# Performance work log

Hardware: AMD Instinct MI355X
Metric: run time of the kernel (lower is better)

The kernel has to match this reference:

```python
import jax, jax.numpy as jnp
import numpy as np

B, D, WIN, SW = 256, 38, 640, 10
S = WIN // SW  # 64 time steps
EPS = 1e-5

def leaky(v):
    return jnp.where(v > 0, v, 0.01 * v)

def _ln(v, g, b):
    mu = v.mean(-1, keepdims=True)
    var = v.var(-1, keepdims=True)
    return g * (v - mu) / jnp.sqrt(var + EPS) + b

def setup_inputs():
    key = jax.random.key(0)
    ks = jax.random.split(key, 24)
    n = lambda k, shp, s=0.05: jax.random.normal(k, shp, jnp.float32) * s
    return {
        'x': jax.random.normal(ks[0], (B, D, WIN), jnp.float32),
        'W1': n(ks[1], (D, 64, SW)), 'b1': n(ks[2], (D, 64)),
        'W2': n(ks[3], (D, 4, 3)), 'b2': n(ks[4], (D, 4)),
        'Wl': n(ks[5], (D, 64, 124)), 'bl': n(ks[6], (D, 64)),
        'Wb1': n(ks[7], (64, 64)), 'bb1': n(ks[8], (64,)),
        'lng': jnp.ones((64,), jnp.float32), 'lnb': jnp.zeros((64,), jnp.float32),
        'Wb2': n(ks[9], (64, 64)), 'bb2': n(ks[10], (64,)),
        'Wq': n(ks[11], (1, 64)), 'bq': n(ks[12], (1,)),
        'Wk': n(ks[13], (D, 64)), 'bk': n(ks[14], (D,)),
        'Wv1': n(ks[15], (D, 32, 64)), 'bv1': n(ks[16], (D, 32)),
        'lnvg': jnp.ones((D, 32), jnp.float32), 'lnvb': jnp.zeros((D, 32), jnp.float32),
        'Wv2': n(ks[17], (D, 32)), 'bv2': n(ks[18], (D,)),
        'Wq2': n(ks[19], (1, 64 * D)), 'bq2': n(ks[20], (1,)),
        'Wk2': n(ks[21], (S, 64 * D)), 'bk2': n(ks[22], (S,)),
    }

def reference(x, W1, b1, W2, b2, Wl, bl, Wb1, bb1, lng, lnb, Wb2, bb2,
              Wq, bq, Wk, bk, Wv1, bv1, lnvg, lnvb, Wv2, bv2, Wq2, bq2, Wk2, bk2):
    Bsz = x.shape[0]
    # FE1: per-channel Conv1d(1,64,k=SW,stride=SW) == window-reshape + per-dim GEMM
    xw = x.reshape(Bsz, D, S, SW)
    f1 = leaky(jnp.einsum('bdsw,dow->bdso', xw, W1) + b1[None, :, None, :])  # [B,D,S,64]
    # FE2: per-channel Conv1d(1,4,k=3,p=1) over the 64 features
    xp = jnp.pad(f1, ((0, 0), (0, 0), (0, 0), (1, 1)))
    win = jnp.stack([xp[..., r:r + 64] for r in range(3)], -1)  # [B,D,S,64,3]
    c = leaky(jnp.einsum('bdstr,dcr->bdsct', win, W2) + b2[None, :, None, :, None])  # [B,D,S,4,64]
    # MaxPool1d(3, stride=2): 64 -> 31
    m = jnp.max(jnp.stack([c[..., s:s + 61:2] for s in range(3)], 0), 0)  # [B,D,S,4,31]
    e = leaky(jnp.einsum('bdsf,dof->bdso', m.reshape(Bsz, D, S, 124), Wl) + bl[None, :, None, :])  # embed [B,D,S,64]
    # BeforeInstanceEncoder (shared), recurrent accumulator == cumsum over time
    h = leaky(_ln(jnp.einsum('bdso,po->bdsp', e, Wb1) + bb1, lng, lnb))
    g = leaky(jnp.einsum('bdsp,qp->bdsq', h, Wb2) + bb2)
    acml = jnp.cumsum(g, axis=2)  # [B,D,S,64]
    wq = jax.nn.sigmoid(jnp.einsum('bdso,o->bds', e, Wq[0]) + bq[0])            # [B,D,S]
    wk = jax.nn.sigmoid(jnp.einsum('bdso,jo->bdsj', acml, Wk) + bk)             # [B,D,S,D]
    att1 = jax.nn.softmax(jnp.einsum('bks,bjsk->bsj', wq, wk) / np.float32(np.sqrt(D)), axis=-1)  # [B,S,D]
    v = leaky(_ln(jnp.einsum('bdso,dho->bdsh', e, Wv1) + bv1[None, :, None, :],
                  lnvg[None, :, None, :], lnvb[None, :, None, :]))
    wv = jax.nn.relu(jnp.einsum('bdsh,dh->bds', v, Wv2) + bv2[None, :, None])   # [B,D,S]
    cont1 = jnp.transpose(wv, (0, 2, 1)) * att1  # [B,S,D]
    contributes1 = cont1[..., None]              # [B,S,D,1]
    output1 = cont1.sum(-1, keepdims=True)       # [B,S,1]
    # bag-level attention over time
    ef = jnp.transpose(e, (0, 2, 1, 3)).reshape(Bsz, S, D * 64)
    wq_a = jax.nn.sigmoid(ef @ Wq2.T + bq2)[..., 0]  # [B,S]
    wk_a = jax.nn.sigmoid(ef @ Wk2.T + bk2)          # [B,S,S]
    att2 = jax.nn.softmax(jnp.einsum('bs,bts->bt', wq_a, wk_a) / np.float32(np.sqrt(WIN)), axis=-1)  # [B,S]
    contributes2 = output1 * att2[..., None]  # [B,S,1]
    output2 = contributes2.sum(1)             # [B,1]
    return (output2, contributes2, contributes1)
```

## Files before the change

### kernel.cpp

```cpp
#include <hip/hip_runtime.h>
#include <math.h>

#define Bv 256
#define Dv 38
#define Sv 64
#define SWv 10
#define EPSv 1e-5f

typedef float f4 __attribute__((ext_vector_type(4)));

__device__ __forceinline__ float leaky(float v){ return v > 0.f ? v : 0.01f*v; }
__device__ __forceinline__ float sigm(float v){ return 1.f/(1.f+expf(-v)); }

__device__ __forceinline__ float wred64(float v){
  #pragma unroll
  for (int off=32; off; off>>=1) v += __shfl_xor(v, off, 64);
  return v;
}
__device__ __forceinline__ float wmax64(float v){
  #pragma unroll
  for (int off=32; off; off>>=1) v = fmaxf(v, __shfl_xor(v, off, 64));
  return v;
}

__global__ __launch_bounds__(256) void k0_pack(
    const float* __restrict__ Wl, const float* __restrict__ W1,
    const float* __restrict__ Wv1, const float* __restrict__ Wb1,
    const float* __restrict__ Wb2, const float* __restrict__ Wk,
    const float* __restrict__ Wk2,
    float* __restrict__ wlT, float* __restrict__ w1T, float* __restrict__ wv1T,
    float* __restrict__ wb1T, float* __restrict__ wb2T, float* __restrict__ wkT,
    float* __restrict__ wk2T)
{
  int idx = blockIdx.x*256 + threadIdx.x;
  if (idx < 330752) {
    int d = idx / 8704, r = idx % 8704;
    int c = r / 1088, rr = r % 1088;
    int q = rr / 68, o = rr % 68;
    int ch = q >> 2, io = q & 3, fi = 4*c + io;
    float v = 0.f;
    if (o < 64 && fi <= 30) v = Wl[d*7936 + o*124 + ch*31 + fi];
    wlT[idx] = v;
  } else if (idx < 356592) {
    int t = idx - 330752;
    int d = t / 680, rr = t % 680;
    int w = rr / 68, o = rr % 68;
    w1T[t] = (o < 64) ? W1[d*640 + o*10 + w] : 0.f;
  } else if (idx < 444144) {
    int t = idx - 356592;
    int d = t / 2304, rr = t % 2304;
    int o = rr / 36, h = rr % 36;
    wv1T[t] = (h < 32) ? Wv1[d*2048 + h*64 + o] : 0.f;
  } else if (idx < 448240) {
    int t = idx - 444144;
    int o = t >> 6, p = t & 63;
    wb1T[t] = Wb1[p*64 + o];
  } else if (idx < 452336) {
    int t = idx - 448240;
    int p = t >> 6, q = t & 63;
    wb2T[t] = Wb2[q*64 + p];
  } else if (idx < 454896) {
    int t = idx - 452336;
    int q = t / 40, k = t % 40;
    wkT[t] = (k < Dv) ? Wk[k*64 + q] : 0.f;
  } else if (idx < 610544) {
    int t = idx - 454896;
    int d = t / 4096, rr = t % 4096;
    int o = rr >> 6, s = rr & 63;
    wk2T[t] = Wk2[s*2432 + d*64 + o];
  }
}

__global__ __launch_bounds__(256, 3) void k1_fe4(
    const float* __restrict__ x,
    const float* __restrict__ w1T_all, const float* __restrict__ b1,
    const float* __restrict__ W2, const float* __restrict__ b2,
    const float* __restrict__ wlT_all, const float* __restrict__ bl,
    const float* __restrict__ Wq, const float* __restrict__ bq,
    const float* __restrict__ wv1T_all, const float* __restrict__ bv1,
    const float* __restrict__ lnvg, const float* __restrict__ lnvb,
    const float* __restrict__ Wv2, const float* __restrict__ bv2,
    const float* __restrict__ Wq2,
    float* __restrict__ e_wsT, float* __restrict__ wq2_ws, float* __restrict__ wv_ws,
    float* __restrict__ wqa_p)
{
  __shared__ float sm[12688];
  const int d  = blockIdx.x >> 7;
  const int b0 = (blockIdx.x & 127) * 2;
  const int tid = threadIdx.x;
  const int z = tid >> 7;
  const int t = tid & 127;
  const int tx = t & 15, ty = t >> 4;
  const int wz = ty >> 2;
  const int bd = (b0 + z)*Dv + d;
  const float bq0 = bq[0];

#define PJ(j) ((j) < 4 ? 4*ty + (j) : 32 + 4*ty + ((j)-4))

  if (tid < 64) {
    sm[12032+tid] = b1[d*64+tid];
    sm[12096+tid] = bl[d*64+tid];
    sm[12160+tid] = Wq[tid];
    sm[12368+tid] = Wq2[d*64+tid];
  } else if (tid < 96) {
    int u = tid-64;
    sm[12240+u]=bv1[d*32+u]; sm[12272+u]=lnvg[d*32+u];
    sm[12304+u]=lnvb[d*32+u]; sm[12336+u]=Wv2[d*32+u];
  } else if (tid < 108) sm[12224+(tid-96)] = W2[d*12+(tid-96)];
  else if (tid < 112)   sm[12236+(tid-108)] = b2[d*4+(tid-108)];

  {
    const f4* s4 = (const f4*)(w1T_all + (size_t)d*680);
    if (tid < 170) ((f4*)&sm[9792])[tid] = s4[tid];
  }
  for (int i = tid; i < 1280; i += 256) {
    int z2 = i / 640, tt = i % 640;
    sm[10472 + z2*680 + (tt%10)*68 + tt/10] =
      x[((size_t)((b0+z2)*Dv + d))*640 + tt];
  }
  const f4* wlsrc = (const f4*)(wlT_all + (size_t)d*8704);
  {
    ((f4*)&sm[8704])[tid] = wlsrc[tid];
    if (tid < 16) ((f4*)&sm[8704])[tid+256] = wlsrc[tid+256];
  }
  __syncthreads();

  float fe[4][8];
  #pragma unroll
  for (int i=0;i<4;++i)
    #pragma unroll
    for (int j=0;j<8;++j) fe[i][j]=0.f;
  #pragma unroll
  for (int w = 0; w < 10; ++w) {
    f4 a   = *(const f4*)&sm[10472 + z*680 + w*68 + 4*tx];
    f4 blo = *(const f4*)&sm[9792 + w*68 + 4*ty];
    f4 bhi = *(const f4*)&sm[9792 + w*68 + 32 + 4*ty];
    #pragma unroll
    for (int i=0;i<4;++i)
      #pragma unroll
      for (int j=0;j<8;++j) fe[i][j] += a[i]*((j<4)?blo[j&3]:bhi[j&3]);
  }
  #pragma unroll
  for (int j=0;j<8;++j) {
    int o = PJ(j);
    float bb = sm[12032+o];
    f4 v = {leaky(fe[0][j]+bb), leaky(fe[1][j]+bb), leaky(fe[2][j]+bb), leaky(fe[3][j]+bb)};
    *(f4*)&sm[z*4352 + o*68 + 4*tx] = v;
  }
  __syncthreads();

  float ea[4][8];
  #pragma unroll
  for (int i=0;i<4;++i)
    #pragma unroll
    for (int j=0;j<8;++j) ea[i][j]=0.f;

  f4 wr0, wr1;
  for (int c = 0; c < 8; ++c) {
    if (c > 0) {
      ((f4*)&sm[8704])[tid] = wr0;
      if (tid < 16) ((f4*)&sm[8704])[tid+256] = wr1;
    }
    {
      int sg = t & 15, io = (t >> 4) & 3, chh = t >> 6;
      int fi = 4*c + io;
      if (fi <= 30) {
        int t0 = 2*fi - 1;
        const float* fsrc = &sm[z*4352];
        f4 v0;
        if (fi == 0) { v0[0]=0.f; v0[1]=0.f; v0[2]=0.f; v0[3]=0.f; }
        else         { v0 = *(const f4*)&fsrc[t0*68 + 4*sg]; }
        f4 v1 = *(const f4*)&fsrc[(t0+1)*68 + 4*sg];
        f4 v2 = *(const f4*)&fsrc[(t0+2)*68 + 4*sg];
        f4 v3 = *(const f4*)&fsrc[(t0+3)*68 + 4*sg];
        f4 v4 = *(const f4*)&fsrc[(t0+4)*68 + 4*sg];
        float* mdst = &sm[9792 + z*1088];
        #pragma unroll
        for (int cc2 = 0; cc2 < 2; ++cc2) {
          int ch = 2*chh + cc2;
          float w0=sm[12224+ch*3], w1=sm[12224+ch*3+1], w2=sm[12224+ch*3+2];
          float bb=sm[12236+ch];
          f4 r;
          #pragma unroll
          for (int e2=0;e2<4;++e2) {
            float ca = bb + v0[e2]*w0 + v1[e2]*w1 + v2[e2]*w2;
            float cb = bb + v1[e2]*w0 + v2[e2]*w1 + v3[e2]*w2;
            float cc = bb + v2[e2]*w0 + v3[e2]*w1 + v4[e2]*w2;
            r[e2] = fmaxf(fmaxf(leaky(ca),leaky(cb)),leaky(cc));
          }
          *(f4*)&mdst[(ch*4+io)*68 + 4*sg] = r;
        }
      }
    }
    if (c < 7) {
      wr0 = wlsrc[(c+1)*272 + tid];
      if (tid < 16) wr1 = wlsrc[(c+1)*272 + 256 + tid];
    }
    __syncthreads();
    {
      const float* ma = &sm[9792 + z*1088];
      #pragma unroll
      for (int q=0;q<16;++q){
        f4 a   = *(const f4*)&ma[q*68+4*tx];
        f4 blo = *(const f4*)&sm[8704 + q*68+4*ty];
        f4 bhi = *(const f4*)&sm[8704 + q*68+32+4*ty];
        #pragma unroll
        for (int i=0;i<4;++i)
          #pragma unroll
          for (int j=0;j<8;++j) ea[i][j] += a[i]*((j<4)?blo[j&3]:bhi[j&3]);
      }
    }
    __syncthreads();
  }

  float ev[4][8];
  #pragma unroll
  for (int i=0;i<4;++i)
    #pragma unroll
    for (int j=0;j<8;++j) ev[i][j] = leaky(ea[i][j] + sm[12096 + PJ(j)]);

  {
    float* erow = e_wsT + (size_t)bd * 4096;
    #pragma unroll
    for (int j=0;j<8;++j) {
      f4 v = {ev[0][j],ev[1][j],ev[2][j],ev[3][j]};
      *(f4*)&erow[PJ(j)*64 + 4*tx] = v;
    }
  }
  #pragma unroll
  for (int j=0;j<8;++j) {
    int o = PJ(j);
    f4 v = {ev[0][j],ev[1][j],ev[2][j],ev[3][j]};
    *(f4*)&sm[z*4352 + o*68 + 4*tx] = v;
  }
  #pragma unroll
  for (int i=0;i<4;++i) {
    float p = 0.f, pa = 0.f;
    #pragma unroll
    for (int j=0;j<8;++j) {
      p  += ev[i][j]*sm[12160 + PJ(j)];
      pa += ev[i][j]*sm[12368 + PJ(j)];
    }
    p += __shfl_xor(p, 16);  p += __shfl_xor(p, 32);
    pa += __shfl_xor(pa, 16); pa += __shfl_xor(pa, 32);
    if ((ty & 3) == 0) {
      sm[11520 + z*128 + wz*64 + 4*tx + i] = p;
      sm[12432 + z*128 + wz*64 + 4*tx + i] = pa;
    }
  }
  {
    const f4* s4 = (const f4*)(wv1T_all + (size_t)d*2304);
    f4 a0 = s4[tid], a1 = s4[tid+256];
    ((f4*)&sm[8704])[tid] = a0;
    ((f4*)&sm[8704])[tid+256] = a1;
    if (tid < 64) ((f4*)&sm[8704])[tid+512] = s4[tid+512];
  }
  __syncthreads();

  if (tid < 128) {
    int z2 = tid >> 6, r = tid & 63;
    float p = sm[11520 + z2*128 + r] + sm[11520 + z2*128 + 64 + r];
    wq2_ws[((size_t)(b0+z2)*64 + r)*Dv + d] = sigm(p + bq0);
    float pa = sm[12432 + z2*128 + r] + sm[12432 + z2*128 + 64 + r];
    wqa_p[((size_t)(b0+z2)*64 + r)*Dv + d] = pa;
  }

  float va[4][4];
  #pragma unroll
  for (int i=0;i<4;++i)
    #pragma unroll
    for (int j=0;j<4;++j) va[i][j]=0.f;
  #pragma unroll 8
  for (int o = 0; o < 64; ++o) {
    f4 a  = *(const f4*)&sm[z*4352 + o*68 + 4*tx];
    f4 bb = *(const f4*)&sm[8704 + o*36 + 4*ty];
    #pragma unroll
    for (int i=0;i<4;++i)
      #pragma unroll
      for (int j=0;j<4;++j) va[i][j] += a[i]*bb[j];
  }
  #pragma unroll
  for (int i=0;i<4;++i)
    #pragma unroll
    for (int j=0;j<4;++j) va[i][j] += sm[12240 + 4*ty + j];

  #pragma unroll
  for (int i=0;i<4;++i) {
    float ps=0.f, pq=0.f;
    #pragma unroll
    for (int j=0;j<4;++j) { ps += va[i][j]; pq += va[i][j]*va[i][j]; }
    ps += __shfl_xor(ps, 16); ps += __shfl_xor(ps, 32);
    pq += __shfl_xor(pq, 16); pq += __shfl_xor(pq, 32);
    if ((ty & 3) == 0) {
      sm[11008 + z*128 + wz*64 + 4*tx + i] = ps;
      sm[11264 + z*128 + wz*64 + 4*tx + i] = pq;
    }
  }
  __syncthreads();
  if (tid < 128) {
    int z2 = tid >> 6, r = tid & 63;
    float s_ = sm[11008 + z2*128 + r] + sm[11008 + z2*128 + 64 + r];
    float q_ = sm[11264 + z2*128 + r] + sm[11264 + z2*128 + 64 + r];
    float mu = s_*(1.f/32.f);
    float vr = q_*(1.f/32.f) - mu*mu;
    sm[11776 + z2*64 + r] = mu;
    sm[11904 + z2*64 + r] = rsqrtf(vr + EPSv);
  }
  __syncthreads();

  #pragma unroll
  for (int i=0;i<4;++i) {
    float mu = sm[11776 + z*64 + 4*tx + i];
    float rs = sm[11904 + z*64 + 4*tx + i];
    float p = 0.f;
    #pragma unroll
    for (int j=0;j<4;++j) {
      int h = 4*ty + j;
      float vh = leaky(sm[12272+h]*(va[i][j]-mu)*rs + sm[12304+h]);
      p += vh*sm[12336+h];
    }
    p += __shfl_xor(p, 16);
    p += __shfl_xor(p, 32);
    if ((ty & 3) == 0) sm[11520 + z*128 + wz*64 + 4*tx + i] = p;
  }
  __syncthreads();
  if (tid < 128) {
    int z2 = tid >> 6, r = tid & 63;
    float p = sm[11520 + z2*128 + r] + sm[11520 + z2*128 + 64 + r];
    wv_ws[((size_t)((b0+z2)*Dv + d))*64 + r] = fmaxf(p + bv2[d], 0.f);
  }
#undef PJ
}

__global__ __launch_bounds__(256) void k2_fused(
    const float* __restrict__ e_wsT,
    const float* __restrict__ wb1T, const float* __restrict__ bb1,
    const float* __restrict__ lng, const float* __restrict__ lnb,
    const float* __restrict__ wb2T, const float* __restrict__ bb2,
    const float* __restrict__ wkT, const float* __restrict__ bk,
    const float* __restrict__ wq2_ws, float* __restrict__ score1)
{
  __shared__ float smem[12864];
  float* bufA = smem;
  float* bufB = smem + 8448;
  float* pts  = smem + 12544;
  float* ptq  = smem + 12704;

  const int tid = threadIdx.x;
  const int tx = tid & 31;
  const int ty = tid >> 5;
  const int lane = tid & 63;
  const int bd0 = blockIdx.x * 2;
  const int bd1 = bd0 + 1;

#define PJ(j) ((j) < 4 ? 4*ty + (j) : 32 + 4*ty + ((j)-4))

  if (tid < 128) { pts[tid] = 0.f; ptq[tid] = 0.f; }

  f4 w2r[4];
  {
    const f4* s4 = (const f4*)wb2T;
    #pragma unroll
    for (int q = 0; q < 4; ++q) w2r[q] = s4[tid + 256*q];
  }

  {
    const f4* Esrc = (const f4*)(e_wsT + (size_t)bd0 * 4096);
    #pragma unroll
    for (int m = 0; m < 8; ++m) {
      int n = tid + 256*m;
      int o = n >> 5, t5 = n & 31;
      int z = t5 >> 4, sg = t5 & 15;
      *(f4*)&bufA[o*132 + z*64 + 4*sg] = Esrc[z*1024 + o*16 + sg];
    }
    const f4* W1s = (const f4*)wb1T;
    #pragma unroll
    for (int m = 0; m < 4; ++m) {
      int n = tid + 256*m;
      ((f4*)bufB)[n] = W1s[n];
    }
  }
  __syncthreads();

  float bb1v[8], lngv[8], lnbv[8], bb2v[8];
  #pragma unroll
  for (int j=0;j<8;++j) {
    int p = PJ(j);
    bb1v[j]=bb1[p]; lngv[j]=lng[p]; lnbv[j]=lnb[p]; bb2v[j]=bb2[p];
  }

  float h[4][8];
  #pragma unroll
  for (int i=0;i<4;++i)
    #pragma unroll
    for (int j=0;j<8;++j) h[i][j]=0.f;
  for (int o = 0; o < 64; ++o) {
    f4 a  = *(const f4*)(bufA + o*132 + 4*tx);
    f4 bl = *(const f4*)(bufB + o*64 + 4*ty);
    f4 bh = *(const f4*)(bufB + o*64 + 32 + 4*ty);
    #pragma unroll
    for (int i=0;i<4;++i)
      #pragma unroll
      for (int j=0;j<8;++j) h[i][j] += a[i]*((j<4)?bl[j&3]:bh[j&3]);
  }
  #pragma unroll
  for (int i=0;i<4;++i)
    #pragma unroll
    for (int j=0;j<8;++j) h[i][j] += bb1v[j];

  #pragma unroll
  for (int i=0;i<4;++i) {
    float ps=0.f, pq=0.f;
    #pragma unroll
    for (int j=0;j<8;++j) { ps += h[i][j]; pq += h[i][j]*h[i][j]; }
    ps += __shfl_xor(ps, 32);
    pq += __shfl_xor(pq, 32);
    if (lane < 32) {
      atomicAdd(&pts[4*tx+i], ps);
      atomicAdd(&ptq[4*tx+i], pq);
    }
  }
  __syncthreads();

  {
    #pragma unroll
    for (int q = 0; q < 4; ++q) ((f4*)bufB)[tid + 256*q] = w2r[q];
  }
  {
    float muv[4], rsv[4];
    #pragma unroll
    for (int i=0;i<4;++i) {
      float s = pts[4*tx+i], q = ptq[4*tx+i];
      float mu = s*(1.f/64.f);
      float va = q*(1.f/64.f) - mu*mu;
      muv[i] = mu; rsv[i] = rsqrtf(va + EPSv);
    }
    #pragma unroll
    for (int j=0;j<8;++j) {
      f4 v;
      #pragma unroll
      for (int i=0;i<4;++i)
        v[i] = leaky(lngv[j]*(h[i][j]-muv[i])*rsv[i] + lnbv[j]);
      *(f4*)&bufA[PJ(j)*132 + 4*tx] = v;
    }
  }
  __syncthreads();

  if (tid < 128) pts[tid] = 0.f;

  float g[4][8];
  #pragma unroll
  for (int i=0;i<4;++i)
    #pragma unroll
    for (int j=0;j<8;++j) g[i][j]=0.f;
  for (int p = 0; p < 64; ++p) {
    f4 a  = *(const f4*)(bufA + p*132 + 4*tx);
    f4 bl = *(const f4*)(bufB + p*64 + 4*ty);
    f4 bh = *(const f4*)(bufB + p*64 + 32 + 4*ty);
    #pragma unroll
    for (int i=0;i<4;++i)
      #pragma unroll
      for (int j=0;j<8;++j) g[i][j] += a[i]*((j<4)?bl[j&3]:bh[j&3]);
  }
  #pragma unroll
  for (int i=0;i<4;++i)
    #pragma unroll
    for (int j=0;j<8;++j) g[i][j] = leaky(g[i][j] + bb2v[j]);

  #pragma unroll
  for (int j=0;j<8;++j) {
    float c0_=g[0][j], c1=c0_+g[1][j], c2=c1+g[2][j], c3=c2+g[3][j];
    float incl = c3;
    #pragma unroll
    for (int dd=1; dd<16; dd<<=1) {
      float t = __shfl_up(incl, dd, 16);
      if ((tid & 15) >= dd) incl += t;
    }
    float ex = incl - c3;
    g[0][j]=ex+c0_; g[1][j]=ex+c1; g[2][j]=ex+c2; g[3][j]=ex+c3;
  }

  float wkr[10];
  #pragma unroll
  for (int n = 0; n < 10; ++n) wkr[n] = wkT[tid + 256*n];
  __syncthreads();

  #pragma unroll
  for (int j=0;j<8;++j) {
    f4 v = {g[0][j], g[1][j], g[2][j], g[3][j]};
    *(f4*)&bufA[PJ(j)*132 + 4*tx] = v;
  }
  #pragma unroll
  for (int n = 0; n < 10; ++n) bufB[tid + 256*n] = wkr[n];
  __syncthreads();

  float u[4][4], u2[4][4];
  #pragma unroll
  for (int i=0;i<4;++i)
    #pragma unroll
    for (int j=0;j<4;++j) { u[i][j]=0.f; u2[i][j]=0.f; }
  for (int q = 0; q < 64; ++q) {
    f4 a   = *(const f4*)(bufA + q*132 + 4*tx);
    f4 b1v = *(const f4*)(bufB + q*40 + 4*ty);
    #pragma unroll
    for (int i=0;i<4;++i)
      #pragma unroll
      for (int j=0;j<4;++j) u[i][j] += a[i]*b1v[j];
    if (ty < 2) {
      f4 b2v = *(const f4*)(bufB + q*40 + 32 + 4*ty);
      #pragma unroll
      for (int i=0;i<4;++i)
        #pragma unroll
        for (int j=0;j<4;++j) u2[i][j] += a[i]*b2v[j];
    }
  }

  const int b0g = bd0/Dv, d0g = bd0%Dv, b1g = bd1/Dv, d1g = bd1%Dv;
  #pragma unroll
  for (int i=0;i<4;++i) {
    int r = 4*tx + i;
    int s = r & 63;
    int bb_ = (r >> 6) ? b1g : b0g;
    const float* wqrow = wq2_ws + ((size_t)bb_*Sv + s)*Dv;
    float p = 0.f;
    #pragma unroll
    for (int j=0;j<4;++j) {
      int k = 4*ty + j;
      p += sigm(u[i][j] + bk[k]) * wqrow[k];
    }
    if (ty < 2) {
      #pragma unroll
      for (int j=0;j<4;++j) {
        int k = 32 + 4*ty + j;
        if (k < Dv) p += sigm(u2[i][j] + bk[k]) * wqrow[k];
      }
    }
    p += __shfl_xor(p, 32);
    if (lane < 32) atomicAdd(&pts[r], p);
  }
  __syncthreads();
  if (tid < 128) {
    float tot = pts[tid];
    int grp = tid >> 6, s = tid & 63;
    int bb_ = grp ? b1g : b0g;
    int dd_ = grp ? d1g : d0g;
    score1[((size_t)bb_*Sv + s)*Dv + dd_] = tot;
  }
#undef PJ
}

__global__ __launch_bounds__(64) void k3_att1(
    const float* __restrict__ score1, const float* __restrict__ wv_ws,
    const float* __restrict__ wqa_p, const float* __restrict__ bq2,
    float* __restrict__ out_c1, float* __restrict__ output1, float* __restrict__ wq_a)
{
  const int blk = blockIdx.x;
  const int b = blk / Sv, s = blk % Sv;
  const int lane = threadIdx.x;

  const float invsq = 0.16222142113076254f;
  float sc = (lane<Dv) ? score1[(b*Sv+s)*Dv+lane]*invsq : -1e30f;
  float mx = wmax64(sc);
  float ex = (lane<Dv) ? expf(sc-mx) : 0.f;
  float den = wred64(ex);
  float att = ex/den;
  float c1 = 0.f;
  if (lane<Dv) {
    c1 = wv_ws[(b*Dv+lane)*Sv+s]*att;
    out_c1[(b*Sv+s)*Dv+lane] = c1;
  }
  float tot = wred64(c1);
  if (lane==0) output1[b*Sv+s] = tot;

  float p = (lane < Dv) ? wqa_p[((size_t)b*Sv + s)*Dv + lane] : 0.f;
  p = wred64(p);
  if (lane==0) wq_a[b*Sv+s] = sigm(p + bq2[0]);
}

__global__ __launch_bounds__(256) void k4_gemm(
    const float* __restrict__ e_wsT, const float* __restrict__ wk2T,
    const float* __restrict__ bk2,
    const float* __restrict__ wq_a, float* __restrict__ score2)
{
  const int b = blockIdx.x;
  const int tid = threadIdx.x;
  const int tx = tid & 15, ty = tid >> 4;
  __shared__ float AsT[64*68];
  __shared__ float BsT[64*68];
  __shared__ float pt[64*17];

  float acc[4][4];
  #pragma unroll
  for (int i=0;i<4;++i)
    #pragma unroll
    for (int j=0;j<4;++j) acc[i][j]=0.f;

  for (int d = 0; d < 38; ++d) {
    const f4* Asrc = (const f4*)(e_wsT + ((size_t)(b*Dv+d))*4096);
    const f4* Bsrc = (const f4*)(wk2T + (size_t)d*4096);
    #pragma unroll
    for (int m = 0; m < 4; ++m) {
      int n = tid + 256*m;
      int o = n >> 4, sg = n & 15;
      *(f4*)&AsT[o*68 + 4*sg] = Asrc[n];
      *(f4*)&BsT[o*68 + 4*sg] = Bsrc[n];
    }
    __syncthreads();
    #pragma unroll 4
    for (int o = 0; o < 64; ++o) {
      f4 a  = *(const f4*)&AsT[o*68 + 4*tx];
      f4 bb = *(const f4*)&BsT[o*68 + 4*ty];
      #pragma unroll
      for (int i=0;i<4;++i)
        #pragma unroll
        for (int j=0;j<4;++j) acc[i][j] += a[i]*bb[j];
    }
    __syncthreads();
  }

  #pragma unroll
  for (int i=0;i<4;++i) {
    float p = 0.f;
    #pragma unroll
    for (int j=0;j<4;++j) {
      int s = 4*ty + j;
      p += sigm(acc[i][j] + bk2[s]) * wq_a[b*Sv + s];
    }
    pt[(4*tx+i)*17 + ty] = p;
  }
  __syncthreads();
  if (tid < 64) {
    float tot = 0.f;
    #pragma unroll
    for (int y=0;y<16;++y) tot += pt[tid*17+y];
    score2[b*Sv + tid] = tot;
  }
}

__global__ __launch_bounds__(64) void k5_final(
    const float* __restrict__ score2, const float* __restrict__ output1,
    float* __restrict__ out)
{
  const int b = blockIdx.x;
  const int lane = threadIdx.x;
  const float inv = 0.039528470752104741f;
  float v = score2[b*Sv+lane]*inv;
  float mx = wmax64(v);
  float ex = expf(v-mx);
  float den = wred64(ex);
  float att = ex/den;
  float c2 = output1[b*Sv+lane]*att;
  out[256 + b*Sv + lane] = c2;
  float tot = wred64(c2);
  if (lane==0) out[b] = tot;
}

extern "C" void kernel_launch(void* const* d_in, const int* in_sizes, int n_in,
                              void* d_out, int out_size, void* d_ws, size_t ws_size,
                              hipStream_t stream)
{
  const float* x    = (const float*)d_in[0];
  const float* W1   = (const float*)d_in[1];
  const float* b1   = (const float*)d_in[2];
  const float* W2   = (const float*)d_in[3];
  const float* b2   = (const float*)d_in[4];
  const float* Wl   = (const float*)d_in[5];
  const float* bl   = (const float*)d_in[6];
  const float* Wb1  = (const float*)d_in[7];
  const float* bb1  = (const float*)d_in[8];
  const float* lng  = (const float*)d_in[9];
  const float* lnb  = (const float*)d_in[10];
  const float* Wb2  = (const float*)d_in[11];
  const float* bb2  = (const float*)d_in[12];
  const float* Wq   = (const float*)d_in[13];
  const float* bq   = (const float*)d_in[14];
  const float* Wk   = (const float*)d_in[15];
  const float* bk   = (const float*)d_in[16];
  const float* Wv1  = (const float*)d_in[17];
  const float* bv1  = (const float*)d_in[18];
  const float* lnvg = (const float*)d_in[19];
  const float* lnvb = (const float*)d_in[20];
  const float* Wv2  = (const float*)d_in[21];
  const float* bv2  = (const float*)d_in[22];
  const float* Wq2  = (const float*)d_in[23];
  const float* bq2  = (const float*)d_in[24];
  const float* Wk2  = (const float*)d_in[25];
  const float* bk2  = (const float*)d_in[26];

  float* ws = (float*)d_ws;
  float* e_wsT = ws;
  float* wq2w  = e_wsT + (size_t)Bv*Dv*Sv*64;
  float* wv_ws = wq2w + (size_t)Bv*Sv*Dv;
  float* sc1   = wv_ws + (size_t)Bv*Dv*Sv;
  float* out1  = sc1 + (size_t)Bv*Sv*Dv;
  float* wqa   = out1 + (size_t)Bv*Sv;
  float* sc2   = wqa + (size_t)Bv*Sv;
  float* wlT   = sc2 + (size_t)Bv*Sv;
  float* w1T   = wlT + 330752;
  float* wv1T  = w1T + 25840;
  float* wqap  = wv1T + 87552;
  float* wb1T  = wqap + (size_t)Bv*Sv*Dv;
  float* wb2T  = wb1T + 4096;
  float* wkT   = wb2T + 4096;
  float* wk2T  = wkT + 2560;

  float* out = (float*)d_out;
  float* out_c1 = out + 256 + Bv*Sv;

  hipLaunchKernelGGL(k0_pack, dim3(2385), dim3(256), 0, stream,
    Wl, W1, Wv1, Wb1, Wb2, Wk, Wk2, wlT, w1T, wv1T, wb1T, wb2T, wkT, wk2T);
  hipLaunchKernelGGL(k1_fe4, dim3(Dv*128), dim3(256), 0, stream,
    x, w1T, b1, W2, b2, wlT, bl, Wq, bq, wv1T, bv1, lnvg, lnvb, Wv2, bv2,
    Wq2, e_wsT, wq2w, wv_ws, wqap);
  hipLaunchKernelGGL(k2_fused, dim3(Bv*Dv/2), dim3(256), 0, stream,
    e_wsT, wb1T, bb1, lng, lnb, wb2T, bb2, wkT, bk, wq2w, sc1);
  hipLaunchKernelGGL(k3_att1, dim3(Bv*Sv), dim3(64), 0, stream,
    sc1, wv_ws, wqap, bq2, out_c1, out1, wqa);
  hipLaunchKernelGGL(k4_gemm, dim3(Bv), dim3(256), 0, stream,
    e_wsT, wk2T, bk2, wqa, sc2);
  hipLaunchKernelGGL(k5_final, dim3(Bv), dim3(64), 0, stream, sc2, out1, out);
}
```

Before: 602.8 us.

## Store embeddings and bag weights in fp16 and use packed dot2 in GEMMs

The embedding tensor e is now written to the workspace in fp16 with an s-major layout, and the Wb1/Wb2/Wk/Wk2 weights are packed as fp16. The k2 and k4 GEMMs load half-precision rows and accumulate through fdot2 (8-element dot products) into fp32. This halves the bytes moved for the large e tensor and the weights, and doubles arithmetic density per instruction. It trades away precision in the attention scores. The k2 cumulative-sum scan was rewritten as a 32-lane shuffle scan to match the new row mapping.

Result: slower. 710.6 us (+17.9%).

```diff
diff --git a/kernel.cpp b/kernel.cpp
--- a/kernel.cpp
+++ b/kernel.cpp
@@ -8,6 +8,9 @@
 #define EPSv 1e-5f
 
 typedef float f4 __attribute__((ext_vector_type(4)));
+typedef _Float16 h2 __attribute__((ext_vector_type(2)));
+typedef _Float16 h4 __attribute__((ext_vector_type(4)));
+typedef _Float16 h8 __attribute__((ext_vector_type(8)));
 
 __device__ __forceinline__ float leaky(float v){ return v > 0.f ? v : 0.01f*v; }
 __device__ __forceinline__ float sigm(float v){ return 1.f/(1.f+expf(-v)); }
@@ -21,6 +24,21 @@
   #pragma unroll
   for (int off=32; off; off>>=1) v = fmaxf(v, __shfl_xor(v, off, 64));
   return v;
+}
+
+__device__ __forceinline__ float dot8(h8 a, h8 b, float c){
+#if __has_builtin(__builtin_amdgcn_fdot2)
+  h2 a0={a[0],a[1]}, a1={a[2],a[3]}, a2={a[4],a[5]}, a3={a[6],a[7]};
+  h2 b0={b[0],b[1]}, b1={b[2],b[3]}, b2={b[4],b[5]}, b3={b[6],b[7]};
+  c = __builtin_amdgcn_fdot2(a0,b0,c,false);
+  c = __builtin_amdgcn_fdot2(a1,b1,c,false);
+  c = __builtin_amdgcn_fdot2(a2,b2,c,false);
+  c = __builtin_amdgcn_fdot2(a3,b3,c,false);
+#else
+  #pragma unroll
+  for (int q=0;q<8;++q) c += (float)a[q]*(float)b[q];
+#endif
+  return c;
 }
 
 __global__ __launch_bounds__(256) void k0_pack(
@@ -29,8 +47,8 @@
     const float* __restrict__ Wb2, const float* __restrict__ Wk,
     const float* __restrict__ Wk2,
     float* __restrict__ wlT, float* __restrict__ w1T, float* __restrict__ wv1T,
-    float* __restrict__ wb1T, float* __restrict__ wb2T, float* __restrict__ wkT,
-    float* __restrict__ wk2T)
+    _Float16* __restrict__ wb1H, _Float16* __restrict__ wb2H,
+    _Float16* __restrict__ wkH, _Float16* __restrict__ wk2H)
 {
   int idx = blockIdx.x*256 + threadIdx.x;
   if (idx < 330752) {
@@ -53,21 +71,17 @@
     wv1T[t] = (h < 32) ? Wv1[d*2048 + h*64 + o] : 0.f;
   } else if (idx < 448240) {
     int t = idx - 444144;
-    int o = t >> 6, p = t & 63;
-    wb1T[t] = Wb1[p*64 + o];
+    wb1H[t] = (_Float16)Wb1[t];
   } else if (idx < 452336) {
     int t = idx - 448240;
-    int p = t >> 6, q = t & 63;
-    wb2T[t] = Wb2[q*64 + p];
+    wb2H[t] = (_Float16)Wb2[t];
   } else if (idx < 454896) {
     int t = idx - 452336;
-    int q = t / 40, k = t % 40;
-    wkT[t] = (k < Dv) ? Wk[k*64 + q] : 0.f;
+    int k = t >> 6, q = t & 63;
+    wkH[t] = (k < Dv) ? (_Float16)Wk[k*64 + q] : (_Float16)0.f;
   } else if (idx < 610544) {
     int t = idx - 454896;
-    int d = t / 4096, rr = t % 4096;
-    int o = rr >> 6, s = rr & 63;
-    wk2T[t] = Wk2[s*2432 + d*64 + o];
+    wk2H[t] = (_Float16)Wk2[t];
   }
 }
 
@@ -81,7 +95,7 @@
     const float* __restrict__ lnvg, const float* __restrict__ lnvb,
     const float* __restrict__ Wv2, const float* __restrict__ bv2,
     const float* __restrict__ Wq2,
-    float* __restrict__ e_wsT, float* __restrict__ wq2_ws, float* __restrict__ wv_ws,
+    _Float16* __restrict__ e_h, float* __restrict__ wq2_ws, float* __restrict__ wv_ws,
     float* __restrict__ wqa_p)
 {
   __shared__ float sm[12688];
@@ -220,11 +234,13 @@
     for (int j=0;j<8;++j) ev[i][j] = leaky(ea[i][j] + sm[12096 + PJ(j)]);
 
   {
-    float* erow = e_wsT + (size_t)bd * 4096;
-    #pragma unroll
-    for (int j=0;j<8;++j) {
-      f4 v = {ev[0][j],ev[1][j],ev[2][j],ev[3][j]};
-      *(f4*)&erow[PJ(j)*64 + 4*tx] = v;
+    _Float16* erow = e_h + (size_t)bd * 4096;
+    #pragma unroll
+    for (int i=0;i<4;++i) {
+      h4 lo = {(_Float16)ev[i][0],(_Float16)ev[i][1],(_Float16)ev[i][2],(_Float16)ev[i][3]};
+      h4 hi = {(_Float16)ev[i][4],(_Float16)ev[i][5],(_Float16)ev[i][6],(_Float16)ev[i][7]};
+      *(h4*)&erow[(4*tx+i)*64 + 4*ty] = lo;
+      *(h4*)&erow[(4*tx+i)*64 + 32 + 4*ty] = hi;
     }
   }
   #pragma unroll
@@ -333,18 +349,18 @@
 }
 
 __global__ __launch_bounds__(256) void k2_fused(
-    const float* __restrict__ e_wsT,
-    const float* __restrict__ wb1T, const float* __restrict__ bb1,
+    const _Float16* __restrict__ e_h,
+    const _Float16* __restrict__ wb1H, const float* __restrict__ bb1,
     const float* __restrict__ lng, const float* __restrict__ lnb,
-    const float* __restrict__ wb2T, const float* __restrict__ bb2,
-    const float* __restrict__ wkT, const float* __restrict__ bk,
+    const _Float16* __restrict__ wb2H, const float* __restrict__ bb2,
+    const _Float16* __restrict__ wkH, const float* __restrict__ bk,
     const float* __restrict__ wq2_ws, float* __restrict__ score1)
 {
-  __shared__ float smem[12864];
-  float* bufA = smem;
-  float* bufB = smem + 8448;
-  float* pts  = smem + 12544;
-  float* ptq  = smem + 12704;
+  __shared__ float smem[7168];
+  _Float16* Ah = (_Float16*)smem;
+  _Float16* Bh = (_Float16*)(smem + 4608);
+  float* pts = smem + 6912;
+  float* ptq = smem + 7040;
 
   const int tid = threadIdx.x;
   const int tx = tid & 31;
@@ -354,30 +370,29 @@
   const int bd1 = bd0 + 1;
 
 #define PJ(j) ((j) < 4 ? 4*ty + (j) : 32 + 4*ty + ((j)-4))
+#define SCAN32(src, inc) { inc = (src); \
+  _Pragma("unroll") \
+  for (int dd=1; dd<32; dd<<=1) { float tt = __shfl_up(inc, dd, 32); if ((tid&31) >= dd) inc += tt; } }
 
   if (tid < 128) { pts[tid] = 0.f; ptq[tid] = 0.f; }
 
-  f4 w2r[4];
+  h8 w2r0, w2r1;
+  { const h8* s = (const h8*)wb2H; w2r0 = s[tid]; w2r1 = s[tid+256]; }
+
   {
-    const f4* s4 = (const f4*)wb2T;
-    #pragma unroll
-    for (int q = 0; q < 4; ++q) w2r[q] = s4[tid + 256*q];
-  }
-
-  {
-    const f4* Esrc = (const f4*)(e_wsT + (size_t)bd0 * 4096);
-    #pragma unroll
-    for (int m = 0; m < 8; ++m) {
-      int n = tid + 256*m;
-      int o = n >> 5, t5 = n & 31;
-      int z = t5 >> 4, sg = t5 & 15;
-      *(f4*)&bufA[o*132 + z*64 + 4*sg] = Esrc[z*1024 + o*16 + sg];
-    }
-    const f4* W1s = (const f4*)wb1T;
+    const h8* Es = (const h8*)(e_h + (size_t)bd0 * 4096);
     #pragma unroll
     for (int m = 0; m < 4; ++m) {
       int n = tid + 256*m;
-      ((f4*)bufB)[n] = W1s[n];
+      int r = n >> 3, og = n & 7;
+      *(h8*)&Ah[r*72 + og*8] = Es[n];
+    }
+    const h8* W1s = (const h8*)wb1H;
+    #pragma unroll
+    for (int m = 0; m < 2; ++m) {
+      int n = tid + 256*m;
+      int r = n >> 3, og = n & 7;
+      *(h8*)&Bh[r*72 + og*8] = W1s[n];
     }
   }
   __syncthreads();
@@ -391,134 +406,150 @@
 
   float h[4][8];
   #pragma unroll
-  for (int i=0;i<4;++i)
-    #pragma unroll
-    for (int j=0;j<8;++j) h[i][j]=0.f;
-  for (int o = 0; o < 64; ++o) {
-    f4 a  = *(const f4*)(bufA + o*132 + 4*tx);
-    f4 bl = *(const f4*)(bufB + o*64 + 4*ty);
-    f4 bh = *(const f4*)(bufB + o*64 + 32 + 4*ty);
-    #pragma unroll
-    for (int i=0;i<4;++i)
-      #pragma unroll
-      for (int j=0;j<8;++j) h[i][j] += a[i]*((j<4)?bl[j&3]:bh[j&3]);
-  }
-  #pragma unroll
-  for (int i=0;i<4;++i)
-    #pragma unroll
-    for (int j=0;j<8;++j) h[i][j] += bb1v[j];
-
-  #pragma unroll
-  for (int i=0;i<4;++i) {
+  for (int m=0;m<4;++m)
+    #pragma unroll
+    for (int j=0;j<8;++j) h[m][j]=0.f;
+  #pragma unroll
+  for (int st = 0; st < 8; ++st) {
+    h8 a[4];
+    #pragma unroll
+    for (int m=0;m<4;++m) a[m] = *(const h8*)&Ah[(tx+32*m)*72 + 8*st];
+    #pragma unroll
+    for (int j=0;j<8;++j) {
+      h8 b = *(const h8*)&Bh[PJ(j)*72 + 8*st];
+      #pragma unroll
+      for (int m=0;m<4;++m) h[m][j] = dot8(a[m], b, h[m][j]);
+    }
+  }
+  #pragma unroll
+  for (int m=0;m<4;++m)
+    #pragma unroll
+    for (int j=0;j<8;++j) h[m][j] += bb1v[j];
+
+  #pragma unroll
+  for (int m=0;m<4;++m) {
     float ps=0.f, pq=0.f;
     #pragma unroll
-    for (int j=0;j<8;++j) { ps += h[i][j]; pq += h[i][j]*h[i][j]; }
+    for (int j=0;j<8;++j) { ps += h[m][j]; pq += h[m][j]*h[m][j]; }
     ps += __shfl_xor(ps, 32);
     pq += __shfl_xor(pq, 32);
-    if (lane < 32) {
-      atomicAdd(&pts[4*tx+i], ps);
-      atomicAdd(&ptq[4*tx+i], pq);
-    }
+    if (lane < 32) { atomicAdd(&pts[tx+32*m], ps); atomicAdd(&ptq[tx+32*m], pq); }
   }
   __syncthreads();
 
   {
-    #pragma unroll
-    for (int q = 0; q < 4; ++q) ((f4*)bufB)[tid + 256*q] = w2r[q];
+    int n = tid, r = n>>3, og = n&7;
+    *(h8*)&Bh[r*72 + og*8] = w2r0;
+    int n2 = tid+256; r = n2>>3; og = n2&7;
+    *(h8*)&Bh[r*72 + og*8] = w2r1;
+  }
+  #pragma unroll
+  for (int m=0;m<4;++m) {
+    int r = tx + 32*m;
+    float s = pts[r], q = ptq[r];
+    float mu = s*(1.f/64.f);
+    float va = q*(1.f/64.f) - mu*mu;
+    float rs = rsqrtf(va + EPSv);
+    h4 lo, hi;
+    #pragma unroll
+    for (int j=0;j<4;++j) lo[j] = (_Float16)leaky(lngv[j]*(h[m][j]-mu)*rs + lnbv[j]);
+    #pragma unroll
+    for (int j=4;j<8;++j) hi[j-4] = (_Float16)leaky(lngv[j]*(h[m][j]-mu)*rs + lnbv[j]);
+    *(h4*)&Ah[r*72 + 4*ty] = lo;
+    *(h4*)&Ah[r*72 + 32 + 4*ty] = hi;
+  }
+  __syncthreads();
+  if (tid < 128) pts[tid] = 0.f;
+
+  float g[4][8];
+  #pragma unroll
+  for (int m=0;m<4;++m)
+    #pragma unroll
+    for (int j=0;j<8;++j) g[m][j]=0.f;
+  #pragma unroll
+  for (int st = 0; st < 8; ++st) {
+    h8 a[4];
+    #pragma unroll
+    for (int m=0;m<4;++m) a[m] = *(const h8*)&Ah[(tx+32*m)*72 + 8*st];
+    #pragma unroll
+    for (int j=0;j<8;++j) {
+      h8 b = *(const h8*)&Bh[PJ(j)*72 + 8*st];
+      #pragma unroll
+      for (int m=0;m<4;++m) g[m][j] = dot8(a[m], b, g[m][j]);
+    }
+  }
+  #pragma unroll
+  for (int m=0;m<4;++m)
+    #pragma unroll
+    for (int j=0;j<8;++j) g[m][j] = leaky(g[m][j] + bb2v[j]);
+
+  #pragma unroll
+  for (int j=0;j<8;++j) {
+    float i0; SCAN32(g[0][j], i0);
+    float tot0 = __shfl(i0, 31, 32);
+    g[0][j] = i0;
+    float i1; SCAN32(g[1][j], i1);
+    g[1][j] = tot0 + i1;
+    float i2; SCAN32(g[2][j], i2);
+    float tot2 = __shfl(i2, 31, 32);
+    g[2][j] = i2;
+    float i3; SCAN32(g[3][j], i3);
+    g[3][j] = tot2 + i3;
+  }
+
+  h8 wk0, wk1;
+  { const h8* s = (const h8*)wkH; wk0 = s[tid]; if (tid < 64) wk1 = s[tid+256]; }
+  __syncthreads();
+
+  #pragma unroll
+  for (int m=0;m<4;++m) {
+    int r = tx + 32*m;
+    h4 lo, hi;
+    #pragma unroll
+    for (int j=0;j<4;++j) lo[j] = (_Float16)g[m][j];
+    #pragma unroll
+    for (int j=4;j<8;++j) hi[j-4] = (_Float16)g[m][j];
+    *(h4*)&Ah[r*72 + 4*ty] = lo;
+    *(h4*)&Ah[r*72 + 32 + 4*ty] = hi;
   }
   {
-    float muv[4], rsv[4];
-    #pragma unroll
-    for (int i=0;i<4;++i) {
-      float s = pts[4*tx+i], q = ptq[4*tx+i];
-      float mu = s*(1.f/64.f);
-      float va = q*(1.f/64.f) - mu*mu;
-      muv[i] = mu; rsv[i] = rsqrtf(va + EPSv);
-    }
-    #pragma unroll
-    for (int j=0;j<8;++j) {
-      f4 v;
-      #pragma unroll
-      for (int i=0;i<4;++i)
-        v[i] = leaky(lngv[j]*(h[i][j]-muv[i])*rsv[i] + lnbv[j]);
-      *(f4*)&bufA[PJ(j)*132 + 4*tx] = v;
-    }
-  }
-  __syncthreads();
-
-  if (tid < 128) pts[tid] = 0.f;
-
-  float g[4][8];
-  #pragma unroll
-  for (int i=0;i<4;++i)
-    #pragma unroll
-    for (int j=0;j<8;++j) g[i][j]=0.f;
-  for (int p = 0; p < 64; ++p) {
-    f4 a  = *(const f4*)(bufA + p*132 + 4*tx);
-    f4 bl = *(const f4*)(bufB + p*64 + 4*ty);
-    f4 bh = *(const f4*)(bufB + p*64 + 32 + 4*ty);
-    #pragma unroll
-    for (int i=0;i<4;++i)
-      #pragma unroll
-      for (int j=0;j<8;++j) g[i][j] += a[i]*((j<4)?bl[j&3]:bh[j&3]);
-  }
-  #pragma unroll
-  for (int i=0;i<4;++i)
-    #pragma unroll
-    for (int j=0;j<8;++j) g[i][j] = leaky(g[i][j] + bb2v[j]);
-
-  #pragma unroll
-  for (int j=0;j<8;++j) {
-    float c0_=g[0][j], c1=c0_+g[1][j], c2=c1+g[2][j], c3=c2+g[3][j];
-    float incl = c3;
-    #pragma unroll
-    for (int dd=1; dd<16; dd<<=1) {
-      float t = __shfl_up(incl, dd, 16);
-      if ((tid & 15) >= dd) incl += t;
-    }
-    float ex = incl - c3;
-    g[0][j]=ex+c0_; g[1][j]=ex+c1; g[2][j]=ex+c2; g[3][j]=ex+c3;
-  }
-
-  float wkr[10];
-  #pragma unroll
-  for (int n = 0; n < 10; ++n) wkr[n] = wkT[tid + 256*n];
-  __syncthreads();
-
-  #pragma unroll
-  for (int j=0;j<8;++j) {
-    f4 v = {g[0][j], g[1][j], g[2][j], g[3][j]};
-    *(f4*)&bufA[PJ(j)*132 + 4*tx] = v;
-  }
-  #pragma unroll
-  for (int n = 0; n < 10; ++n) bufB[tid + 256*n] = wkr[n];
+    int n = tid, r = n>>3, og = n&7;
+    *(h8*)&Bh[r*72 + og*8] = wk0;
+    if (tid < 64) { int n2 = tid+256; r = n2>>3; og = n2&7; *(h8*)&Bh[r*72 + og*8] = wk1; }
+  }
   __syncthreads();
 
   float u[4][4], u2[4][4];
   #pragma unroll
-  for (int i=0;i<4;++i)
-    #pragma unroll
-    for (int j=0;j<4;++j) { u[i][j]=0.f; u2[i][j]=0.f; }
-  for (int q = 0; q < 64; ++q) {
-    f4 a   = *(const f4*)(bufA + q*132 + 4*tx);
-    f4 b1v = *(const f4*)(bufB + q*40 + 4*ty);
-    #pragma unroll
-    for (int i=0;i<4;++i)
-      #pragma unroll
-      for (int j=0;j<4;++j) u[i][j] += a[i]*b1v[j];
+  for (int m=0;m<4;++m)
+    #pragma unroll
+    for (int j=0;j<4;++j) { u[m][j]=0.f; u2[m][j]=0.f; }
+  #pragma unroll
+  for (int st = 0; st < 8; ++st) {
+    h8 a[4];
+    #pragma unroll
+    for (int m=0;m<4;++m) a[m] = *(const h8*)&Ah[(tx+32*m)*72 + 8*st];
+    #pragma unroll
+    for (int j=0;j<4;++j) {
+      h8 b = *(const h8*)&Bh[(4*ty+j)*72 + 8*st];
+      #pragma unroll
+      for (int m=0;m<4;++m) u[m][j] = dot8(a[m], b, u[m][j]);
+    }
     if (ty < 2) {
-      f4 b2v = *(const f4*)(bufB + q*40 + 32 + 4*ty);
-      #pragma unroll
-      for (int i=0;i<4;++i)
+      #pragma unroll
+      for (int j=0;j<4;++j) {
+        h8 b = *(const h8*)&Bh[(32+4*ty+j)*72 + 8*st];
         #pragma unroll
-        for (int j=0;j<4;++j) u2[i][j] += a[i]*b2v[j];
-    }
-  }
-
-  const int b0g = bd0/Dv, d0g = bd0%Dv, b1g = bd1/Dv, d1g = bd1%Dv;
-  #pragma unroll
-  for (int i=0;i<4;++i) {
-    int r = 4*tx + i;
+        for (int m=0;m<4;++m) u2[m][j] = dot8(a[m], b, u2[m][j]);
+      }
+    }
+  }
+
+  const int b0g = bd0/Dv, b1g = bd1/Dv;
+  const int d0g = bd0%Dv, d1g = bd1%Dv;
+  #pragma unroll
+  for (int m=0;m<4;++m) {
+    int r = tx + 32*m;
     int s = r & 63;
     int bb_ = (r >> 6) ? b1g : b0g;
     const float* wqrow = wq2_ws + ((size_t)bb_*Sv + s)*Dv;
@@ -526,13 +557,13 @@
     #pragma unroll
     for (int j=0;j<4;++j) {
       int k = 4*ty + j;
-      p += sigm(u[i][j] + bk[k]) * wqrow[k];
+      p += sigm(u[m][j] + bk[k]) * wqrow[k];
     }
     if (ty < 2) {
       #pragma unroll
       for (int j=0;j<4;++j) {
         int k = 32 + 4*ty + j;
-        if (k < Dv) p += sigm(u2[i][j] + bk[k]) * wqrow[k];
+        if (k < Dv) p += sigm(u2[m][j] + bk[k]) * wqrow[k];
       }
     }
     p += __shfl_xor(p, 32);
@@ -547,6 +578,7 @@
     score1[((size_t)bb_*Sv + s)*Dv + dd_] = tot;
   }
 #undef PJ
+#undef SCAN32
 }
 
 __global__ __launch_bounds__(64) void k3_att1(
@@ -578,55 +610,59 @@
 }
 
 __global__ __launch_bounds__(256) void k4_gemm(
-    const float* __restrict__ e_wsT, const float* __restrict__ wk2T,
+    const _Float16* __restrict__ e_h, const _Float16* __restrict__ wk2H,
     const float* __restrict__ bk2,
     const float* __restrict__ wq_a, float* __restrict__ score2)
 {
   const int b = blockIdx.x;
   const int tid = threadIdx.x;
   const int tx = tid & 15, ty = tid >> 4;
-  __shared__ float AsT[64*68];
-  __shared__ float BsT[64*68];
-  __shared__ float pt[64*17];
+  __shared__ float smem[5696];
+  _Float16* Ah = (_Float16*)smem;
+  _Float16* Bh = (_Float16*)(smem + 2304);
+  float* pt = smem + 4608;
 
   float acc[4][4];
   #pragma unroll
-  for (int i=0;i<4;++i)
-    #pragma unroll
-    for (int j=0;j<4;++j) acc[i][j]=0.f;
+  for (int m=0;m<4;++m)
+    #pragma unroll
+    for (int n=0;n<4;++n) acc[m][n]=0.f;
 
   for (int d = 0; d < 38; ++d) {
-    const f4* Asrc = (const f4*)(e_wsT + ((size_t)(b*Dv+d))*4096);
-    const f4* Bsrc = (const f4*)(wk2T + (size_t)d*4096);
-    #pragma unroll
-    for (int m = 0; m < 4; ++m) {
-      int n = tid + 256*m;
-      int o = n >> 4, sg = n & 15;
-      *(f4*)&AsT[o*68 + 4*sg] = Asrc[n];
-      *(f4*)&BsT[o*68 + 4*sg] = Bsrc[n];
+    const h8* Asrc = (const h8*)(e_h + ((size_t)(b*Dv+d))*4096);
+    const h8* Bsrc = (const h8*)wk2H;
+    #pragma unroll
+    for (int m2 = 0; m2 < 2; ++m2) {
+      int n = tid + 256*m2;
+      int r = n >> 3, og = n & 7;
+      *(h8*)&Ah[r*72 + og*8] = Asrc[n];
+      *(h8*)&Bh[r*72 + og*8] = Bsrc[(size_t)r*304 + d*8 + og];
     }
     __syncthreads();
-    #pragma unroll 4
-    for (int o = 0; o < 64; ++o) {
-      f4 a  = *(const f4*)&AsT[o*68 + 4*tx];
-      f4 bb = *(const f4*)&BsT[o*68 + 4*ty];
-      #pragma unroll
-      for (int i=0;i<4;++i)
+    #pragma unroll
+    for (int st = 0; st < 8; ++st) {
+      h8 a[4];
+      #pragma unroll
+      for (int m=0;m<4;++m) a[m] = *(const h8*)&Ah[(tx+16*m)*72 + 8*st];
+      #pragma unroll
+      for (int n=0;n<4;++n) {
+        h8 bb = *(const h8*)&Bh[(ty+16*n)*72 + 8*st];
         #pragma unroll
-        for (int j=0;j<4;++j) acc[i][j] += a[i]*bb[j];
+        for (int m=0;m<4;++m) acc[m][n] = dot8(a[m], bb, acc[m][n]);
+      }
     }
     __syncthreads();
   }
 
   #pragma unroll
-  for (int i=0;i<4;++i) {
+  for (int m=0;m<4;++m) {
     float p = 0.f;
     #pragma unroll
-    for (int j=0;j<4;++j) {
-      int s = 4*ty + j;
-      p += sigm(acc[i][j] + bk2[s]) * wq_a[b*Sv + s];
-    }
-    pt[(4*tx+i)*17 + ty] = p;
+    for (int n=0;n<4;++n) {
+      int s = ty + 16*n;
+      p += sigm(acc[m][n] + bk2[s]) * wq_a[b*Sv + s];
+    }
+    pt[(tx+16*m)*17 + ty] = p;
   }
   __syncthreads();
   if (tid < 64) {
@@ -688,8 +724,8 @@
   const float* bk2  = (const float*)d_in[26];
 
   float* ws = (float*)d_ws;
-  float* e_wsT = ws;
-  float* wq2w  = e_wsT + (size_t)Bv*Dv*Sv*64;
+  _Float16* e_h = (_Float16*)ws;
+  float* wq2w  = ws + 19922944;
   float* wv_ws = wq2w + (size_t)Bv*Sv*Dv;
   float* sc1   = wv_ws + (size_t)Bv*Dv*Sv;
   float* out1  = sc1 + (size_t)Bv*Sv*Dv;
@@ -699,24 +735,24 @@
   float* w1T   = wlT + 330752;
   float* wv1T  = w1T + 25840;
   float* wqap  = wv1T + 87552;
-  float* wb1T  = wqap + (size_t)Bv*Sv*Dv;
-  float* wb2T  = wb1T + 4096;
-  float* wkT   = wb2T + 4096;
-  float* wk2T  = wkT + 2560;
+  _Float16* wb1H = (_Float16*)(wqap + (size_t)Bv*Sv*Dv);
+  _Float16* wb2H = wb1H + 4096;
+  _Float16* wkH  = wb2H + 4096;
+  _Float16* wk2H = wkH + 2560;
 
   float* out = (float*)d_out;
   float* out_c1 = out + 256 + Bv*Sv;
 
   hipLaunchKernelGGL(k0_pack, dim3(2385), dim3(256), 0, stream,
-    Wl, W1, Wv1, Wb1, Wb2, Wk, Wk2, wlT, w1T, wv1T, wb1T, wb2T, wkT, wk2T);
+    Wl, W1, Wv1, Wb1, Wb2, Wk, Wk2, wlT, w1T, wv1T, wb1H, wb2H, wkH, wk2H);
   hipLaunchKernelGGL(k1_fe4, dim3(Dv*128), dim3(256), 0, stream,
     x, w1T, b1, W2, b2, wlT, bl, Wq, bq, wv1T, bv1, lnvg, lnvb, Wv2, bv2,
-    Wq2, e_wsT, wq2w, wv_ws, wqap);
+    Wq2, e_h, wq2w, wv_ws, wqap);
   hipLaunchKernelGGL(k2_fused, dim3(Bv*Dv/2), dim3(256), 0, stream,
-    e_wsT, wb1T, bb1, lng, lnb, wb2T, bb2, wkT, bk, wq2w, sc1);
+    e_h, wb1H, bb1, lng, lnb, wb2H, bb2, wkH, bk, wq2w, sc1);
   hipLaunchKernelGGL(k3_att1, dim3(Bv*Sv), dim3(64), 0, stream,
     sc1, wv_ws, wqap, bq2, out_c1, out1, wqa);
   hipLaunchKernelGGL(k4_gemm, dim3(Bv), dim3(256), 0, stream,
-    e_wsT, wk2T, bk2, wqa, sc2);
+    e_h, wk2H, bk2, wqa, sc2);
   hipLaunchKernelGGL(k5_final, dim3(Bv), dim3(64), 0, stream, sc2, out1, out);
 }
```
